# Kernel tuning notes

Hardware: AMD Instinct MI355X
Metric: run time of the kernel (lower is better)

Reference implementation:

```python
import jax, jax.numpy as jnp
import numpy as np

P = 16            # decode steps == n_process
M = 4             # number of physical nodes
CAPACITY = [4, 4, 4, 4]
B = 4096          # batch
S = 16            # n_process (sequence length)
G = 128           # gnn_dim
E = 256           # n_embed
H = 512           # n_hidden
CLIP = 10.0       # clip_logits
MASK_PENALTY = 1e8


def setup_inputs() -> dict:
    key = jax.random.key(0)
    ks = jax.random.split(key, 16)
    u = lambda k, shape: jax.random.uniform(k, shape, jnp.float32, -0.08, 0.08)
    return {
        "x": jax.random.normal(ks[0], (B, S, G), jnp.float32),
        "emb_W": u(ks[1], (E, G)),                 # embedding Linear (no bias)
        "enc_Wih": u(ks[2], (4 * H, E)),           # encoder LSTM (gate order i,f,g,o)
        "enc_Whh": u(ks[3], (4 * H, H)),
        "enc_b": u(ks[4], (4 * H,)),               # b_ih + b_hh folded into one bias
        "dec_Wih": u(ks[5], (4 * H, E)),           # decoder LSTM
        "dec_Whh": u(ks[6], (4 * H, H)),
        "dec_b": u(ks[7], (4 * H,)),
        "Wq2": u(ks[8], (H, H)),                   # pointer W_q2
        "bq2": u(ks[9], (H,)),
        "Wref2": u(ks[10], (H, H)),                # pointer W_ref2 (conv1d k=1 == linear)
        "bref2": u(ks[11], (H,)),
        "Vec2": u(ks[12], (H,)),
        "dec_input0": u(ks[13], (E,)),             # learned initial decoder input
    }


def lstm_cell(x, h, c, Wih, Whh, b):
    g = x @ Wih.T + h @ Whh.T + b
    i, f, gg, o = jnp.split(g, 4, axis=-1)
    c = jax.nn.sigmoid(f) * c + jax.nn.sigmoid(i) * jnp.tanh(gg)
    h = jax.nn.sigmoid(o) * jnp.tanh(c)
    return h, c


def reference(x, emb_W, enc_Wih, enc_Whh, enc_b, dec_Wih, dec_Whh, dec_b,
              Wq2, bq2, Wref2, bref2, Vec2, dec_input0):
    Bx, Sx, _ = x.shape
    emb = x @ emb_W.T                                  # (B,S,E)

    # ---- encoder LSTM over the sequence ----
    def enc_step(carry, xt):
        h, c = carry
        h, c = lstm_cell(xt, h, c, enc_Wih, enc_Whh, enc_b)
        return (h, c), h

    h0 = jnp.zeros((Bx, H), emb.dtype)
    (h, c), enc_hs = jax.lax.scan(enc_step, (h0, h0), jnp.swapaxes(emb, 0, 1))
    ref = jnp.swapaxes(enc_hs, 0, 1)                   # (B,S,H)

    # W_ref2 conv1d(k=1) applied to ref is step-invariant: hoist out of the loop
    u2 = jnp.einsum('bsh,oh->bso', ref, Wref2) + bref2  # (B,S,H)

    dec0 = jnp.broadcast_to(dec_input0, (Bx, E))
    mask0 = jnp.zeros((Bx, Sx), emb.dtype)

    def dec_step(carry, _):
        h, c, din, mask = carry
        h, c = lstm_cell(din, h, c, dec_Wih, dec_Whh, dec_b)
        qp = h @ Wq2.T + bq2                           # (B,H)
        t = CLIP * jnp.tanh(qp[:, None, :] + u2)       # (B,S,H)
        logits = jnp.einsum('h,bsh->bs', Vec2, t) - MASK_PENALTY * mask
        log_p = jax.nn.log_softmax(logits, axis=-1)    # (B,S)
        nxt = jnp.argmax(log_p, axis=1)                # greedy node selector
        din = jnp.take_along_axis(emb, nxt[:, None, None], axis=1)[:, 0, :]
        mask = mask + jax.nn.one_hot(nxt, Sx, dtype=mask.dtype)
        return (h, c, din, mask), (nxt, log_p)

    _, (pis, log_ps) = jax.lax.scan(dec_step, (h, c, dec0, mask0), None, length=P)
    pi = jnp.swapaxes(pis, 0, 1)                       # (B,P)
    log_ps = jnp.swapaxes(log_ps, 0, 1)                # (B,P,S)

    # log-likelihood of the chosen tour
    ll = jnp.take_along_axis(log_ps, pi[:, :, None], axis=2)[..., 0].sum(axis=1)

    # __get_mapping: node id per step depends only on the capacity vector
    nodes = jnp.asarray(np.repeat(np.arange(M), np.asarray(CAPACITY))[:P], jnp.int32)
    rows = jnp.arange(Bx)
    mapping = jnp.full((Bx, P), -1, jnp.int32)
    mapping = mapping.at[rows[:, None], pi].set(jnp.broadcast_to(nodes, (Bx, P)))
    return mapping, ll
```

## Files before the change

kernel.cpp:

```cpp
#include <hip/hip_runtime.h>
#include <cstddef>

#define Bsz  4096
#define Sseq 16
#define Gdim 128
#define Edim 256
#define Hdim 512
#define H4   2048
#define Psteps 16
#define BK   16

typedef short bfrag8 __attribute__((ext_vector_type(8)));
typedef float f32x4  __attribute__((ext_vector_type(4)));

__device__ __forceinline__ void split3(float f, unsigned short& h,
                                       unsigned short& m, unsigned short& l) {
    unsigned u = __float_as_uint(f);
    h = (unsigned short)(u >> 16);
    float r1 = f - __uint_as_float(u & 0xffff0000u);
    unsigned u1 = __float_as_uint(r1);
    m = (unsigned short)(u1 >> 16);
    float r2 = r1 - __uint_as_float(u1 & 0xffff0000u);
    l = (unsigned short)(__float_as_uint(r2) >> 16);
}

__global__ void fold_kernel(const float* __restrict__ encWih,
                            const float* __restrict__ encWhh,
                            const float* __restrict__ enc_b,
                            const float* __restrict__ decWih,
                            const float* __restrict__ decWhh,
                            const float* __restrict__ dec_b,
                            const float* __restrict__ embW,
                            const float* __restrict__ dec0,
                            unsigned short* __restrict__ encEh,
                            unsigned short* __restrict__ encEm,
                            unsigned short* __restrict__ encEl,
                            unsigned short* __restrict__ encWh,
                            unsigned short* __restrict__ encWm,
                            unsigned short* __restrict__ encWl,
                            unsigned short* __restrict__ decEh,
                            unsigned short* __restrict__ decEm,
                            unsigned short* __restrict__ decEl,
                            unsigned short* __restrict__ decWh,
                            unsigned short* __restrict__ decWm,
                            unsigned short* __restrict__ decWl,
                            float* __restrict__ encBI, float* __restrict__ decBI,
                            float* __restrict__ v0bI) {
    __shared__ float rE[Edim], rD[Edim];
    const int o = blockIdx.x;
    const int gate = o >> 9, j = o & 511;
    const int c = j * 4 + gate;
    const int g = threadIdx.x;
    rE[g]        = encWih[(size_t)o * Edim + g];
    rE[g + Gdim] = encWih[(size_t)o * Edim + g + Gdim];
    rD[g]        = decWih[(size_t)o * Edim + g];
    rD[g + Gdim] = decWih[(size_t)o * Edim + g + Gdim];
    __syncthreads();

    float se = 0.f, sd = 0.f;
#pragma unroll 8
    for (int e = 0; e < Edim; ++e) {
        float w = embW[e * Gdim + g];
        se += rE[e] * w;
        sd += rD[e] * w;
    }
    unsigned short h, m, l;
    split3(se, h, m, l);
    encEh[(size_t)c * Gdim + g] = h; encEm[(size_t)c * Gdim + g] = m;
    encEl[(size_t)c * Gdim + g] = l;
    split3(sd, h, m, l);
    decEh[(size_t)c * Gdim + g] = h; decEm[(size_t)c * Gdim + g] = m;
    decEl[(size_t)c * Gdim + g] = l;
    for (int k = g; k < Hdim; k += Gdim) {
        split3(encWhh[(size_t)o * Hdim + k], h, m, l);
        encWh[(size_t)c * Hdim + k] = h; encWm[(size_t)c * Hdim + k] = m;
        encWl[(size_t)c * Hdim + k] = l;
        split3(decWhh[(size_t)o * Hdim + k], h, m, l);
        decWh[(size_t)c * Hdim + k] = h; decWm[(size_t)c * Hdim + k] = m;
        decWl[(size_t)c * Hdim + k] = l;
    }
    if (g == 0) {
        encBI[c] = enc_b[o];
        decBI[c] = dec_b[o];
        float s = dec_b[o];
        for (int e = 0; e < Edim; ++e) s += rD[e] * dec0[e];
        v0bI[c] = s;
    }
}

__global__ __launch_bounds__(256) void fold_proj(
    const float* __restrict__ Wr, const float* __restrict__ Wq,
    unsigned short* __restrict__ rWh, unsigned short* __restrict__ rWm,
    unsigned short* __restrict__ rWl,
    unsigned short* __restrict__ qWh, unsigned short* __restrict__ qWm,
    unsigned short* __restrict__ qWl) {
    const int o = blockIdx.x;
    const float* src = blockIdx.y ? Wq : Wr;
    unsigned short* ph = blockIdx.y ? qWh : rWh;
    unsigned short* pm = blockIdx.y ? qWm : rWm;
    unsigned short* pl = blockIdx.y ? qWl : rWl;
    for (int k = threadIdx.x; k < Hdim; k += 256) {
        unsigned short h, m, l;
        split3(src[(size_t)o * Hdim + k], h, m, l);
        ph[(size_t)o * Hdim + k] = h;
        pm[(size_t)o * Hdim + k] = m;
        pl[(size_t)o * Hdim + k] = l;
    }
}

__global__ __launch_bounds__(512) void gates_mfma(
    const unsigned short* __restrict__ Wh1, const unsigned short* __restrict__ Wm1,
    const unsigned short* __restrict__ Wl1, int K1,
    const float* __restrict__ X, int ldx,
    const int* __restrict__ gather, int gmul,
    const unsigned short* __restrict__ Wh2, const unsigned short* __restrict__ Wm2,
    const unsigned short* __restrict__ Wl2, int K2,
    const float* __restrict__ Hin,
    const float* __restrict__ biasI,
    const float* __restrict__ c_in, float* __restrict__ h_out,
    float* __restrict__ c_out, int czero)
{
    __shared__ __align__(16) unsigned short wlds[2][3 * 4096];

    const int tid = threadIdx.x;
    const int wv = tid >> 6, lane = tid & 63;
    const int lm = lane & 15, quad = lane >> 4;
    const int c0 = blockIdx.y * 128;
    const int mB0 = blockIdx.x * 128;

    const int mrow = mB0 + wv * 16 + lm;

    const int srow = wv * 16 + (lane >> 2);
    const int sqs = (lane & 3) ^ ((srow >> 1) & 3);
    const size_t roff1 = (size_t)(c0 + srow) * K1 + (size_t)(sqs * 8);
    const size_t roff2 = (size_t)(c0 + srow) * K2 + (size_t)(sqs * 8);

    const float* xr = nullptr;
    const float* hr = nullptr;
    if (X) {
        size_t off = (size_t)mrow * ldx;
        if (gather) off += (size_t)gather[mrow] * gmul;
        xr = X + off;
    }
    if (Hin) hr = Hin + (size_t)mrow * K2;

    int boffW[8];
#pragma unroll
    for (int tn = 0; tn < 8; ++tn) {
        const int r = tn * 16 + lm;
        boffW[tn] = r * 32 + ((quad ^ ((r >> 1) & 3)) * 8);
    }

    auto stage = [&](int kcN, int buf) {
        const bool nX = kcN < K1;
        const int kb = nX ? kcN : kcN - K1;
        unsigned short* lb = &wlds[buf][wv * 512];
        const unsigned short* gh = (nX ? Wh1 + roff1 : Wh2 + roff2) + kb;
        const unsigned short* gm = (nX ? Wm1 + roff1 : Wm2 + roff2) + kb;
        const unsigned short* gl = (nX ? Wl1 + roff1 : Wl2 + roff2) + kb;
        __builtin_amdgcn_global_load_lds(
            (const __attribute__((address_space(1))) void*)gh,
            (__attribute__((address_space(3))) void*)(lb), 16, 0, 0);
        __builtin_amdgcn_global_load_lds(
            (const __attribute__((address_space(1))) void*)gm,
            (__attribute__((address_space(3))) void*)(lb + 4096), 16, 0, 0);
        __builtin_amdgcn_global_load_lds(
            (const __attribute__((address_space(1))) void*)gl,
            (__attribute__((address_space(3))) void*)(lb + 8192), 16, 0, 0);
    };

    f32x4 acc[8];
#pragma unroll
    for (int i = 0; i < 8; ++i) acc[i] = (f32x4){0.f, 0.f, 0.f, 0.f};

    const int KT = K1 + K2;
    stage(0, 0);
    int cur = 0;

    for (int kc = 0; kc < KT; kc += 32) {
        __syncthreads();
        if (kc + 32 < KT) stage(kc + 32, cur ^ 1);

        const bool inX = kc < K1;
        const int kk = (inX ? kc : kc - K1) + quad * 8;

        const float* p = (inX ? xr : hr) + kk;
        float a8[8];
        *(float4*)&a8[0] = *(const float4*)(p);
        *(float4*)&a8[4] = *(const float4*)(p + 4);
        bfrag8 bh, bm, bl;
#pragma unroll
        for (int j = 0; j < 8; ++j) {
            unsigned short h, m, l;
            split3(a8[j], h, m, l);
            bh[j] = (short)h; bm[j] = (short)m; bl[j] = (short)l;
        }

        const unsigned short* bufp = wlds[cur];
#pragma unroll
        for (int hh = 0; hh < 2; ++hh) {
            bfrag8 ah[4], am4[4], al[4];
#pragma unroll
            for (int t = 0; t < 4; ++t) {
                const int tn = hh * 4 + t;
                ah[t]  = *(const bfrag8*)(bufp + boffW[tn]);
                am4[t] = *(const bfrag8*)(bufp + 4096 + boffW[tn]);
                al[t]  = *(const bfrag8*)(bufp + 8192 + boffW[tn]);
            }
#pragma unroll
            for (int t = 0; t < 4; ++t) {
                const int tn = hh * 4 + t;
                f32x4 c = acc[tn];
                c = __builtin_amdgcn_mfma_f32_16x16x32_bf16(ah[t], bl, c, 0, 0, 0);
                c = __builtin_amdgcn_mfma_f32_16x16x32_bf16(al[t], bh, c, 0, 0, 0);
                c = __builtin_amdgcn_mfma_f32_16x16x32_bf16(am4[t], bm, c, 0, 0, 0);
                c = __builtin_amdgcn_mfma_f32_16x16x32_bf16(ah[t], bm, c, 0, 0, 0);
                c = __builtin_amdgcn_mfma_f32_16x16x32_bf16(am4[t], bh, c, 0, 0, 0);
                c = __builtin_amdgcn_mfma_f32_16x16x32_bf16(ah[t], bh, c, 0, 0, 0);
                acc[tn] = c;
            }
        }
        cur ^= 1;
    }

#pragma unroll
    for (int tn = 0; tn < 8; ++tn) {
        const int nb = c0 + tn * 16 + quad * 4;
        float4 bb = *(const float4*)(biasI + nb);
        const int j = nb >> 2;
        const size_t idx = (size_t)mrow * Hdim + j;
        float gi = acc[tn][0] + bb.x;
        float gf = acc[tn][1] + bb.y;
        float gg = acc[tn][2] + bb.z;
        float go = acc[tn][3] + bb.w;
        float si = 1.f / (1.f + expf(-gi));
        float sf = 1.f / (1.f + expf(-gf));
        float so = 1.f / (1.f + expf(-go));
        float co = czero ? 0.f : c_in[idx];
        float cn = si * tanhf(gg) + sf * co;
        c_out[idx] = cn;
        h_out[idx] = so * tanhf(cn);
    }
}

__global__ __launch_bounds__(256) void proj_mfma(
    const unsigned short* __restrict__ Wh, const unsigned short* __restrict__ Wm,
    const unsigned short* __restrict__ Wl,
    const float* __restrict__ A,
    const float* __restrict__ bias,
    float* __restrict__ C, int ldc)
{
    __shared__ __align__(16) unsigned short wlds[2][3 * 2048];
    __shared__ __align__(16) float alds[2][64 * 32];

    const int tid = threadIdx.x;
    const int wv = tid >> 6, lane = tid & 63;
    const int lm = lane & 15, quad = lane >> 4;
    const int nB0 = blockIdx.y * 64;
    const int mB0 = blockIdx.x * 64;

    const int rw = tid >> 2;
    const int sqw = (tid & 3) ^ ((rw >> 1) & 3);
    const size_t wroff = (size_t)(nB0 + rw) * Hdim + (size_t)(sqw * 8);

    const int asw = ((lane & 7) ^ (lane >> 3)) * 4;
    const float* asrc[2];
#pragma unroll
    for (int i = 0; i < 2; ++i) {
        const int r = i * 32 + wv * 8 + (lane >> 3);
        asrc[i] = A + (size_t)(mB0 + r) * Hdim + asw;
    }

    int boffW[4];
#pragma unroll
    for (int tn = 0; tn < 4; ++tn) {
        const int r = tn * 16 + lm;
        boffW[tn] = r * 32 + ((quad ^ ((r >> 1) & 3)) * 8);
    }
    const int ra = wv * 16 + lm;
    const int boffA1 = ra * 32 + (((2 * quad)     ^ (lm & 7)) << 2);
    const int boffA2 = ra * 32 + (((2 * quad + 1) ^ (lm & 7)) << 2);

    auto stage = [&](int kb, int buf) {
        unsigned short* lb0 = &wlds[buf][wv * 512];
        __builtin_amdgcn_global_load_lds(
            (const __attribute__((address_space(1))) void*)(Wh + wroff + kb),
            (__attribute__((address_space(3))) void*)(lb0), 16, 0, 0);
        __builtin_amdgcn_global_load_lds(
            (const __attribute__((address_space(1))) void*)(Wm + wroff + kb),
            (__attribute__((address_space(3))) void*)(lb0 + 2048), 16, 0, 0);
        __builtin_amdgcn_global_load_lds(
            (const __attribute__((address_space(1))) void*)(Wl + wroff + kb),
            (__attribute__((address_space(3))) void*)(lb0 + 4096), 16, 0, 0);
#pragma unroll
        for (int i = 0; i < 2; ++i) {
            float* lb = &alds[buf][(i * 32 + wv * 8) * 32];
            __builtin_amdgcn_global_load_lds(
                (const __attribute__((address_space(1))) void*)(asrc[i] + kb),
                (__attribute__((address_space(3))) void*)lb, 16, 0, 0);
        }
    };

    f32x4 acc[4];
#pragma unroll
    for (int i = 0; i < 4; ++i) acc[i] = (f32x4){0.f, 0.f, 0.f, 0.f};

    stage(0, 0);
    int cur = 0;

    for (int kc = 0; kc < Hdim; kc += 32) {
        __syncthreads();
        if (kc + 32 < Hdim) stage(kc + 32, cur ^ 1);

        const float* abuf = alds[cur];
        float a8[8];
        *(float4*)&a8[0] = *(const float4*)(abuf + boffA1);
        *(float4*)&a8[4] = *(const float4*)(abuf + boffA2);
        bfrag8 bh, bm, bl;
#pragma unroll
        for (int j = 0; j < 8; ++j) {
            unsigned short h, m, l;
            split3(a8[j], h, m, l);
            bh[j] = (short)h; bm[j] = (short)m; bl[j] = (short)l;
        }

        const unsigned short* bufp = wlds[cur];
#pragma unroll
        for (int tn = 0; tn < 4; ++tn) {
            bfrag8 ah  = *(const bfrag8*)(bufp + boffW[tn]);
            bfrag8 am4 = *(const bfrag8*)(bufp + 2048 + boffW[tn]);
            bfrag8 al  = *(const bfrag8*)(bufp + 4096 + boffW[tn]);
            f32x4 c = acc[tn];
            c = __builtin_amdgcn_mfma_f32_16x16x32_bf16(ah,  bl, c, 0, 0, 0);
            c = __builtin_amdgcn_mfma_f32_16x16x32_bf16(al,  bh, c, 0, 0, 0);
            c = __builtin_amdgcn_mfma_f32_16x16x32_bf16(am4, bm, c, 0, 0, 0);
            c = __builtin_amdgcn_mfma_f32_16x16x32_bf16(ah,  bm, c, 0, 0, 0);
            c = __builtin_amdgcn_mfma_f32_16x16x32_bf16(am4, bh, c, 0, 0, 0);
            c = __builtin_amdgcn_mfma_f32_16x16x32_bf16(ah,  bh, c, 0, 0, 0);
            acc[tn] = c;
        }
        cur ^= 1;
    }

    const int m = mB0 + wv * 16 + lm;
#pragma unroll
    for (int tn = 0; tn < 4; ++tn) {
        const int n = nB0 + tn * 16 + quad * 4;
        float4 bb = *(const float4*)(bias + n);
        float4 o;
        o.x = acc[tn][0] + bb.x;
        o.y = acc[tn][1] + bb.y;
        o.z = acc[tn][2] + bb.z;
        o.w = acc[tn][3] + bb.w;
        *(float4*)(C + (size_t)m * ldc + n) = o;
    }
}

__global__ __launch_bounds__(256) void attn_step(const float* __restrict__ qp,
                                                 const float* __restrict__ u2,
                                                 const float* __restrict__ Vec2,
                                                 float* __restrict__ mask,
                                                 float* __restrict__ ll_ws,
                                                 int* __restrict__ nxt,
                                                 float* __restrict__ out_map,
                                                 float* __restrict__ out_ll,
                                                 int step, int node) {
    const int b = blockIdx.x;
    __shared__ float qpS[Hdim];
    __shared__ float vS[Hdim];
    __shared__ float logitS[Sseq];
    const int tid = threadIdx.x;
    qpS[tid]       = qp[(size_t)b * Hdim + tid];
    qpS[tid + 256] = qp[(size_t)b * Hdim + 256 + tid];
    vS[tid]        = Vec2[tid];
    vS[tid + 256]  = Vec2[256 + tid];
    __syncthreads();

    const int wave = tid >> 6, lane = tid & 63;
    for (int si = 0; si < 4; ++si) {
        int s = wave * 4 + si;
        const float* u2p = u2 + ((size_t)b * Sseq + s) * Hdim;
        float sum = 0.f;
#pragma unroll
        for (int i = 0; i < 8; ++i) {
            int hh = lane + i * 64;
            sum += vS[hh] * tanhf(qpS[hh] + u2p[hh]);
        }
        for (int off = 32; off > 0; off >>= 1) sum += __shfl_down(sum, off);
        if (lane == 0) {
            float pen = step ? mask[b * Sseq + s] * 1e8f : 0.f;
            logitS[s] = 10.f * sum - pen;
        }
    }
    __syncthreads();

    if (tid == 0) {
        float mx = logitS[0];
        int am = 0;
        for (int s = 1; s < Sseq; ++s)
            if (logitS[s] > mx) { mx = logitS[s]; am = s; }
        float se = 0.f;
        for (int s = 0; s < Sseq; ++s) se += expf(logitS[s] - mx);
        float lp = -logf(se);
        float llv = (step ? ll_ws[b] : 0.f) + lp;
        ll_ws[b] = llv;
        out_ll[b] = llv;
        nxt[b] = am;
        if (step == 0) {
            for (int s = 0; s < Sseq; ++s) mask[b * Sseq + s] = (s == am) ? 1.f : 0.f;
        } else {
            mask[b * Sseq + am] += 1.f;
        }
        out_map[b * Sseq + am] = (float)node;
    }
}

extern "C" void kernel_launch(void* const* d_in, const int* in_sizes, int n_in,
                              void* d_out, int out_size, void* d_ws, size_t ws_size,
                              hipStream_t stream) {
    const float* x       = (const float*)d_in[0];
    const float* emb_W   = (const float*)d_in[1];
    const float* enc_Wih = (const float*)d_in[2];
    const float* enc_Whh = (const float*)d_in[3];
    const float* enc_b   = (const float*)d_in[4];
    const float* dec_Wih = (const float*)d_in[5];
    const float* dec_Whh = (const float*)d_in[6];
    const float* dec_b   = (const float*)d_in[7];
    const float* Wq2     = (const float*)d_in[8];
    const float* bq2     = (const float*)d_in[9];
    const float* Wref2   = (const float*)d_in[10];
    const float* bref2   = (const float*)d_in[11];
    const float* Vec2    = (const float*)d_in[12];
    const float* dec0    = (const float*)d_in[13];

    float* ws      = (float*)d_ws;
    float* u2      = ws;
    float* h0      = u2 + (size_t)Bsz * Sseq * Hdim;
    float* c0      = h0 + (size_t)Bsz * Hdim;
    float* h1      = c0 + (size_t)Bsz * Hdim;
    float* c1      = h1 + (size_t)Bsz * Hdim;
    float* qp      = c1 + (size_t)Bsz * Hdim;
    float* mask    = qp + (size_t)Bsz * Hdim;
    float* ll      = mask + (size_t)Bsz * Sseq;
    int*   nxt     = (int*)(ll + Bsz);
    float* encBI   = (float*)(nxt + Bsz);
    float* decBI   = encBI + H4;
    float* v0bI    = decBI + H4;
    unsigned short* us = (unsigned short*)(v0bI + H4);
    unsigned short* encEh = us;                       us += (size_t)H4 * Gdim;
    unsigned short* encEm = us;                       us += (size_t)H4 * Gdim;
    unsigned short* encEl = us;                       us += (size_t)H4 * Gdim;
    unsigned short* encWh = us;                       us += (size_t)H4 * Hdim;
    unsigned short* encWm = us;                       us += (size_t)H4 * Hdim;
    unsigned short* encWl = us;                       us += (size_t)H4 * Hdim;
    unsigned short* decEh = us;                       us += (size_t)H4 * Gdim;
    unsigned short* decEm = us;                       us += (size_t)H4 * Gdim;
    unsigned short* decEl = us;                       us += (size_t)H4 * Gdim;
    unsigned short* decWh = us;                       us += (size_t)H4 * Hdim;
    unsigned short* decWm = us;                       us += (size_t)H4 * Hdim;
    unsigned short* decWl = us;                       us += (size_t)H4 * Hdim;
    unsigned short* prWh = us;                        us += (size_t)Hdim * Hdim;
    unsigned short* prWm = us;                        us += (size_t)Hdim * Hdim;
    unsigned short* prWl = us;                        us += (size_t)Hdim * Hdim;
    unsigned short* pqWh = us;                        us += (size_t)Hdim * Hdim;
    unsigned short* pqWm = us;                        us += (size_t)Hdim * Hdim;
    unsigned short* pqWl = us;                        us += (size_t)Hdim * Hdim;

    float* out_map = (float*)d_out;
    float* out_ll  = out_map + (size_t)Bsz * Psteps;

    static const int nodes[Psteps] = {0,0,0,0, 1,1,1,1, 2,2,2,2, 3,3,3,3};

    fold_kernel<<<H4, Gdim, 0, stream>>>(enc_Wih, enc_Whh, enc_b,
                                         dec_Wih, dec_Whh, dec_b,
                                         emb_W, dec0,
                                         encEh, encEm, encEl, encWh, encWm, encWl,
                                         decEh, decEm, decEl, decWh, decWm, decWl,
                                         encBI, decBI, v0bI);
    fold_proj<<<dim3(Hdim, 2), 256, 0, stream>>>(Wref2, Wq2,
                                                 prWh, prWm, prWl,
                                                 pqWh, pqWm, pqWl);

    const dim3 gBig(32, 16);
    const dim3 gPr(64, 8);

    for (int t = 0; t < Sseq; ++t) {
        float* ho = (t & 1) ? h0 : h1;
        float* co = (t & 1) ? c0 : c1;
        const float* hi = (t & 1) ? h1 : h0;
        const float* ci = (t & 1) ? c1 : c0;
        if (t == 0) {
            gates_mfma<<<gBig, 512, 0, stream>>>(
                encEh, encEm, encEl, Gdim,
                x, Sseq * Gdim, nullptr, 0,
                nullptr, nullptr, nullptr, 0, nullptr,
                encBI, ci, ho, co, 1);
        } else {
            gates_mfma<<<gBig, 512, 0, stream>>>(
                encEh, encEm, encEl, Gdim,
                x + t * Gdim, Sseq * Gdim, nullptr, 0,
                encWh, encWm, encWl, Hdim, hi,
                encBI, ci, ho, co, 0);
        }
        proj_mfma<<<gPr, 256, 0, stream>>>(prWh, prWm, prWl, ho, bref2,
                                           u2 + (size_t)t * Hdim, Sseq * Hdim);
    }

    for (int p = 0; p < Psteps; ++p) {
        const int u = Sseq + p;
        float* ho = (u & 1) ? h0 : h1;
        float* co = (u & 1) ? c0 : c1;
        const float* hi = (u & 1) ? h1 : h0;
        const float* ci = (u & 1) ? c1 : c0;
        if (p == 0) {
            gates_mfma<<<gBig, 512, 0, stream>>>(
                nullptr, nullptr, nullptr, 0,
                nullptr, 0, nullptr, 0,
                decWh, decWm, decWl, Hdim, hi,
                v0bI, ci, ho, co, 0);
        } else {
            gates_mfma<<<gBig, 512, 0, stream>>>(
                decEh, decEm, decEl, Gdim,
                x, Sseq * Gdim, nxt, Gdim,
                decWh, decWm, decWl, Hdim, hi,
                decBI, ci, ho, co, 0);
        }
        proj_mfma<<<gPr, 256, 0, stream>>>(pqWh, pqWm, pqWl, ho, bq2,
                                           qp, Hdim);
        attn_step<<<Bsz, 256, 0, stream>>>(qp, u2, Vec2, mask, ll, nxt,
                                           out_map, out_ll, p, nodes[p]);
    }
}
```

Before: 3.231 ms.

## Batch encoder ref projection into one launch over stored hidden sequence

Stores every encoder hidden state in a per-timestep workspace buffer and runs the W_ref2 projection once over all 16 timesteps with a larger grid, instead of launching it after each encoder step. The u2 layout changes from batch-major to step-major, and the attention kernel's indexing is updated to match. This removes 15 small launches and gives the projection a larger, better-filled GEMM. It costs more workspace and only takes effect when the workspace is large enough, otherwise it falls back to the per-step path.

```diff
diff --git a/kernel.cpp b/kernel.cpp
--- a/kernel.cpp
+++ b/kernel.cpp
@@ -379,7 +379,7 @@
     const int wave = tid >> 6, lane = tid & 63;
     for (int si = 0; si < 4; ++si) {
         int s = wave * 4 + si;
-        const float* u2p = u2 + ((size_t)b * Sseq + s) * Hdim;
+        const float* u2p = u2 + ((size_t)s * Bsz + b) * Hdim;
         float sum = 0.f;
 #pragma unroll
         for (int i = 0; i < 8; ++i) {
@@ -433,14 +433,16 @@
     const float* Vec2    = (const float*)d_in[12];
     const float* dec0    = (const float*)d_in[13];
 
+    const size_t BH = (size_t)Bsz * Hdim;
+
     float* ws      = (float*)d_ws;
     float* u2      = ws;
     float* h0      = u2 + (size_t)Bsz * Sseq * Hdim;
-    float* c0      = h0 + (size_t)Bsz * Hdim;
-    float* h1      = c0 + (size_t)Bsz * Hdim;
-    float* c1      = h1 + (size_t)Bsz * Hdim;
-    float* qp      = c1 + (size_t)Bsz * Hdim;
-    float* mask    = qp + (size_t)Bsz * Hdim;
+    float* c0      = h0 + BH;
+    float* h1      = c0 + BH;
+    float* c1      = h1 + BH;
+    float* qp      = c1 + BH;
+    float* mask    = qp + BH;
     float* ll      = mask + (size_t)Bsz * Sseq;
     int*   nxt     = (int*)(ll + Bsz);
     float* encBI   = (float*)(nxt + Bsz);
@@ -465,6 +467,9 @@
     unsigned short* pqWh = us;                        us += (size_t)Hdim * Hdim;
     unsigned short* pqWm = us;                        us += (size_t)Hdim * Hdim;
     unsigned short* pqWl = us;                        us += (size_t)Hdim * Hdim;
+    float* hseq = (float*)us;
+    const size_t need = ((char*)(hseq + (size_t)Sseq * BH)) - (char*)d_ws;
+    const bool batched = (ws_size >= need);
 
     float* out_map = (float*)d_out;
     float* out_ll  = out_map + (size_t)Bsz * Psteps;
@@ -483,11 +488,13 @@
 
     const dim3 gBig(32, 16);
     const dim3 gPr(64, 8);
+    const dim3 gPrB(1024, 8);
 
     for (int t = 0; t < Sseq; ++t) {
-        float* ho = (t & 1) ? h0 : h1;
+        float* ho = batched ? (hseq + (size_t)t * BH) : ((t & 1) ? h0 : h1);
         float* co = (t & 1) ? c0 : c1;
-        const float* hi = (t & 1) ? h1 : h0;
+        const float* hi = batched ? (hseq + (size_t)(t - 1) * BH)
+                                  : ((t & 1) ? h1 : h0);
         const float* ci = (t & 1) ? c1 : c0;
         if (t == 0) {
             gates_mfma<<<gBig, 512, 0, stream>>>(
@@ -502,15 +509,23 @@
                 encWh, encWm, encWl, Hdim, hi,
                 encBI, ci, ho, co, 0);
         }
-        proj_mfma<<<gPr, 256, 0, stream>>>(prWh, prWm, prWl, ho, bref2,
-                                           u2 + (size_t)t * Hdim, Sseq * Hdim);
+        if (!batched) {
+            proj_mfma<<<gPr, 256, 0, stream>>>(prWh, prWm, prWl, ho, bref2,
+                                               u2 + (size_t)t * BH, Hdim);
+        }
+    }
+    if (batched) {
+        proj_mfma<<<gPrB, 256, 0, stream>>>(prWh, prWm, prWl, hseq, bref2,
+                                            u2, Hdim);
     }
 
     for (int p = 0; p < Psteps; ++p) {
         const int u = Sseq + p;
         float* ho = (u & 1) ? h0 : h1;
         float* co = (u & 1) ? c0 : c1;
-        const float* hi = (u & 1) ? h1 : h0;
+        const float* hi;
+        if (p == 0) hi = batched ? (hseq + (size_t)(Sseq - 1) * BH) : h0;
+        else        hi = (u & 1) ? h1 : h0;
         const float* ci = (u & 1) ? c1 : c0;
         if (p == 0) {
             gates_mfma<<<gBig, 512, 0, stream>>>(
```

Measured after the change: 3.258 ms. Within noise of the previous version (+0.8%).
